# Kernel tuning notes

Measured on AMD Instinct MI355X. Metric: run time of the kernel, lower is better.

The kernel has to match this reference:

```python
import jax, jax.numpy as jnp
import numpy as np


def setup_inputs() -> dict:
    key = jax.random.key(0)
    ks = jax.random.split(key, 11)
    b, c, h, w = 16, 64, 16, 16
    F = 64  # num_filters
    O = 64  # num_outputs
    d_in = 2 * (c + 1)  # 130: concat of two (feature + coord) vectors
    s = 0.05
    return {
        "x_img": jax.random.normal(ks[0], (b, c, h, w), dtype=jnp.float32),
        "Wg0": jax.random.normal(ks[1], (F, d_in), dtype=jnp.float32) * s,
        "bg0": jax.random.normal(ks[2], (F,), dtype=jnp.float32) * s,
        "Wg1": jax.random.normal(ks[3], (F, F), dtype=jnp.float32) * s,
        "bg1": jax.random.normal(ks[4], (F,), dtype=jnp.float32) * s,
        "Wg2": jax.random.normal(ks[5], (F, F), dtype=jnp.float32) * s,
        "bg2": jax.random.normal(ks[6], (F,), dtype=jnp.float32) * s,
        "Wp": jax.random.normal(ks[7], (F, F), dtype=jnp.float32) * s,
        "bp": jax.random.normal(ks[8], (F,), dtype=jnp.float32) * s,
        "Wo": jax.random.normal(ks[9], (O, F), dtype=jnp.float32) * s,
        "bo": jax.random.normal(ks[10], (O,), dtype=jnp.float32) * s,
    }


def reference(x_img, Wg0, bg0, Wg1, bg1, Wg2, bg2, Wp, bp, Wo, bo):
    b, c, h, w = x_img.shape
    L = h * w
    # [b, L, c]: flatten spatial, move channels last
    feats = x_img.reshape(b, c, L).transpose(0, 2, 1)
    # append 1-d coordinate feature -> [b, L, c+1]
    coord = jnp.broadcast_to(
        jnp.arange(L, dtype=feats.dtype).reshape(1, L, 1), (b, L, 1)
    )
    feats = jnp.concatenate([feats, coord], axis=2)
    # pairwise broadcast-concat: pair[b, p, q] = [feats[b, q], feats[b, p]]
    d = feats.shape[-1]
    x_i = jnp.broadcast_to(feats[:, None, :, :], (b, L, L, d))
    x_j = jnp.broadcast_to(feats[:, :, None, :], (b, L, L, d))
    pair = jnp.concatenate([x_i, x_j], axis=3)  # [b, L, L, 2*(c+1)]
    # shared g-MLP (3 layers, ReLU)
    out = jax.nn.relu(jnp.einsum("bpqd,fd->bpqf", pair, Wg0) + bg0)
    out = jax.nn.relu(jnp.einsum("bpqf,gf->bpqg", out, Wg1) + bg1)
    out = jax.nn.relu(jnp.einsum("bpqf,gf->bpqg", out, Wg2) + bg2)
    # sum-reduce over both pair dims -> [b, F]
    out = out.sum(axis=(1, 2))
    # f-network
    out = jax.nn.relu(out @ Wp.T + bp)
    out = out @ Wo.T + bo
    return out
```

## Files before the change

### kernel.cpp

```cpp
#include <hip/hip_runtime.h>


typedef short s8v __attribute__((ext_vector_type(8)));
typedef float f4v __attribute__((ext_vector_type(4)));

#define LDYB 72

__device__ __forceinline__ short bfr(float v) {
  return __builtin_bit_cast(short, (__bf16)v);
}
__device__ __forceinline__ unsigned pkbf(float a, float b) {
  unsigned lo = (unsigned short)__builtin_bit_cast(unsigned short, (__bf16)a);
  unsigned hi = (unsigned short)__builtin_bit_cast(unsigned short, (__bf16)b);
  return lo | (hi << 16);
}
__device__ __forceinline__ f4v relu4(f4v v) {
  f4v z = {0.f, 0.f, 0.f, 0.f};
  return __builtin_elementwise_max(v, z);
}
__device__ __forceinline__ s8v cvt8(f4v a, f4v b) {
  s8v r;
  r[0] = bfr(a[0]); r[1] = bfr(a[1]); r[2] = bfr(a[2]); r[3] = bfr(a[3]);
  r[4] = bfr(b[0]); r[5] = bfr(b[1]); r[6] = bfr(b[2]); r[7] = bfr(b[3]);
  return r;
}
__device__ __forceinline__ f4v ldf4(const float* p) {
  return *(const f4v*)p;
}

__global__ __launch_bounds__(256) void k_pre(
    const float* __restrict__ x, const float* __restrict__ Wg0,
    const float* __restrict__ bg0, float* __restrict__ Ag,
    float* __restrict__ Bg, float* __restrict__ Sg) {
  __shared__ float ws[64 * 131];
  __shared__ float xs[64 * 17];

  const int t = threadIdx.x;
  const int b = blockIdx.x >> 4;
  const int l0 = (blockIdx.x & 15) * 16;

  if (blockIdx.x == 0) {
    for (int i = t; i < 16 * 64; i += 256) Sg[i] = 0.f;
  }
  for (int i = t; i < 64 * 130; i += 256) {
    int f = i / 130, d = i - f * 130;
    ws[f * 131 + d] = Wg0[i];
  }
  for (int i = t; i < 64 * 16; i += 256) {
    int ch = i >> 4, li = i & 15;
    xs[ch * 17 + li] = x[b * 16384 + ch * 256 + l0 + li];
  }
  __syncthreads();

  const int f = t & 63;
  const int w = t >> 6;
  float accA[4] = {0.f, 0.f, 0.f, 0.f};
  float accB[4] = {0.f, 0.f, 0.f, 0.f};
  for (int d = 0; d < 64; ++d) {
    float wa = ws[f * 131 + d];
    float wb = ws[f * 131 + 65 + d];
#pragma unroll
    for (int i = 0; i < 4; ++i) {
      float xv = xs[d * 17 + w + 4 * i];
      accA[i] += xv * wa;
      accB[i] += xv * wb;
    }
  }
  const float wca = ws[f * 131 + 64];
  const float wcb = ws[f * 131 + 129];
  const float bias = bg0[f];
#pragma unroll
  for (int i = 0; i < 4; ++i) {
    int l = l0 + w + 4 * i;
    Ag[(b * 256 + l) * 64 + f] = accA[i] + (float)l * wca;
    Bg[(b * 256 + l) * 64 + f] = accB[i] + (float)l * wcb + bias;
  }
}

__global__ __launch_bounds__(256, 2) void k_main(
    const float* __restrict__ Ag, const float* __restrict__ Bg,
    const float* __restrict__ Wg1, const float* __restrict__ bg1,
    const float* __restrict__ Wg2, const float* __restrict__ bg2,
    float* __restrict__ Sg) {
  __shared__ __align__(16) short Ys[4][16 * LDYB];
  __shared__ float Sblk[64];

  const int t = threadIdx.x;
  const int wid = t >> 6;
  const int lane = t & 63;
  const int mm = lane & 15;
  const int quad = lane >> 4;
  const int b = blockIdx.y;
  const int qg = blockIdx.x & 3;
  const int p0 = (blockIdx.x >> 2) * 32;
  const int q0 = (qg * 4 + wid) * 16;

  if (t < 64) Sblk[t] = 0.f;

  const float* Arow = Ag + (b * 256 + q0 + mm) * 64;
  f4v af0 = ldf4(Arow + quad * 8);
  f4v af1 = ldf4(Arow + quad * 8 + 4);
  f4v af2 = ldf4(Arow + 32 + quad * 8);
  f4v af3 = ldf4(Arow + 36 + quad * 8);

  s8v W1f[4][2], W2f[4][2];
  f4v c1i[4], c2i[4];
#pragma unroll
  for (int gt = 0; gt < 4; ++gt) {
    c1i[gt] = ldf4(bg1 + gt * 16 + quad * 4);
    c2i[gt] = ldf4(bg2 + gt * 16 + quad * 4);
#pragma unroll
    for (int kh = 0; kh < 2; ++kh) {
      const float* r1 = Wg1 + (gt * 16 + mm) * 64 + kh * 32 + quad * 8;
      const float* r2 = Wg2 + (gt * 16 + mm) * 64 + kh * 32 + quad * 8;
      s8v w1, w2;
#pragma unroll
      for (int j = 0; j < 8; ++j) { w1[j] = bfr(r1[j]); w2[j] = bfr(r2[j]); }
      W1f[gt][kh] = w1;
      W2f[gt][kh] = w2;
    }
  }
  __syncthreads();

  short* Yw = Ys[wid];
  const float* Bb = Bg + (b * 256 + p0) * 64;
  f4v cs[4] = {{0.f,0.f,0.f,0.f},{0.f,0.f,0.f,0.f},
               {0.f,0.f,0.f,0.f},{0.f,0.f,0.f,0.f}};

  f4v bq0 = ldf4(Bb + quad * 8);
  f4v bq1 = ldf4(Bb + quad * 8 + 4);
  f4v bq2 = ldf4(Bb + 32 + quad * 8);
  f4v bq3 = ldf4(Bb + 36 + quad * 8);

  for (int ip = 0; ip < 32; ++ip) {
    const float* Bn = Bb + ((ip < 31) ? ip + 1 : 31) * 64;
    f4v bn0 = ldf4(Bn + quad * 8);
    f4v bn1 = ldf4(Bn + quad * 8 + 4);
    f4v bn2 = ldf4(Bn + 32 + quad * 8);
    f4v bn3 = ldf4(Bn + 36 + quad * 8);

    s8v x0 = cvt8(relu4(af0 + bq0), relu4(af1 + bq1));
    s8v x1 = cvt8(relu4(af2 + bq2), relu4(af3 + bq3));

#pragma unroll
    for (int gt = 0; gt < 4; ++gt) {
      f4v a = c1i[gt];
      a = __builtin_amdgcn_mfma_f32_16x16x32_bf16(W1f[gt][0], x0, a, 0, 0, 0);
      a = __builtin_amdgcn_mfma_f32_16x16x32_bf16(W1f[gt][1], x1, a, 0, 0, 0);
      a = relu4(a);
      unsigned d0 = pkbf(a[0], a[1]);
      unsigned d1 = pkbf(a[2], a[3]);
      *(uint2*)&Yw[mm * LDYB + gt * 16 + quad * 4] = make_uint2(d0, d1);
    }

    s8v y0 = *(const s8v*)&Yw[mm * LDYB + quad * 8];
    s8v y1 = *(const s8v*)&Yw[mm * LDYB + 32 + quad * 8];

#pragma unroll
    for (int ot = 0; ot < 4; ++ot) {
      f4v a = c2i[ot];
      a = __builtin_amdgcn_mfma_f32_16x16x32_bf16(W2f[ot][0], y0, a, 0, 0, 0);
      a = __builtin_amdgcn_mfma_f32_16x16x32_bf16(W2f[ot][1], y1, a, 0, 0, 0);
      cs[ot] += relu4(a);
    }

    bq0 = bn0; bq1 = bn1; bq2 = bn2; bq3 = bn3;
  }

#pragma unroll
  for (int ot = 0; ot < 4; ++ot) {
#pragma unroll
    for (int r = 0; r < 4; ++r) {
      float v = cs[ot][r];
      v += __shfl_xor(v, 1);
      v += __shfl_xor(v, 2);
      v += __shfl_xor(v, 4);
      v += __shfl_xor(v, 8);
      if (mm == 0) atomicAdd(&Sblk[ot * 16 + quad * 4 + r], v);
    }
  }
  __syncthreads();
  if (t < 64) atomicAdd(&Sg[b * 64 + t], Sblk[t]);
}

__global__ __launch_bounds__(64) void k_final(
    const float* __restrict__ S, const float* __restrict__ Wp,
    const float* __restrict__ bp, const float* __restrict__ Wo,
    const float* __restrict__ bo, float* __restrict__ out) {
  __shared__ float sv[64], tv[64];
  const int b = blockIdx.x, t = threadIdx.x;
  sv[t] = S[b * 64 + t];
  __syncthreads();
  float acc = bp[t];
  for (int g = 0; g < 64; ++g) acc += sv[g] * Wp[t * 64 + g];
  tv[t] = fmaxf(acc, 0.f);
  __syncthreads();
  float o = bo[t];
  for (int f = 0; f < 64; ++f) o += tv[f] * Wo[t * 64 + f];
  out[b * 64 + t] = o;
}

extern "C" void kernel_launch(void* const* d_in, const int* in_sizes, int n_in,
                              void* d_out, int out_size, void* d_ws, size_t ws_size,
                              hipStream_t stream) {
  const float* x   = (const float*)d_in[0];
  const float* Wg0 = (const float*)d_in[1];
  const float* bg0 = (const float*)d_in[2];
  const float* Wg1 = (const float*)d_in[3];
  const float* bg1 = (const float*)d_in[4];
  const float* Wg2 = (const float*)d_in[5];
  const float* bg2 = (const float*)d_in[6];
  const float* Wp  = (const float*)d_in[7];
  const float* bp  = (const float*)d_in[8];
  const float* Wo  = (const float*)d_in[9];
  const float* bo  = (const float*)d_in[10];
  float* out = (float*)d_out;

  float* Ag = (float*)d_ws;
  float* Bg = Ag + 16 * 256 * 64;
  float* Sg = Bg + 16 * 256 * 64;

  k_pre<<<256, 256, 0, stream>>>(x, Wg0, bg0, Ag, Bg, Sg);
  k_main<<<dim3(32, 16), 256, 0, stream>>>(Ag, Bg, Wg1, bg1, Wg2, bg2, Sg);
  k_final<<<16, 64, 0, stream>>>(Sg, Wp, bp, Wo, bo, out);
}
```

Measured before the change: 119.1 us.

## Halve per-block p range, stage B rows in LDS, raise occupancy

Each k_main block now covers 16 p rows instead of 32, so the grid doubles to 1024 blocks. The block's 16 B rows are loaded once into shared memory and read from LDS inside the loop, replacing the per-iteration global prefetch. Launch bounds rise to 4 blocks per SM to allow more waves in flight, and the weight loads are vectorised. The trade-off is twice the redundant weight/A loading and twice as many global atomics, plus tighter register limits that could cause spills.

```diff
diff --git a/kernel.cpp b/kernel.cpp
--- a/kernel.cpp
+++ b/kernel.cpp
@@ -77,12 +77,13 @@
   }
 }
 
-__global__ __launch_bounds__(256, 2) void k_main(
+__global__ __launch_bounds__(256, 4) void k_main(
     const float* __restrict__ Ag, const float* __restrict__ Bg,
     const float* __restrict__ Wg1, const float* __restrict__ bg1,
     const float* __restrict__ Wg2, const float* __restrict__ bg2,
     float* __restrict__ Sg) {
   __shared__ __align__(16) short Ys[4][16 * LDYB];
+  __shared__ __align__(16) float Bs[16 * 64];
   __shared__ float Sblk[64];
 
   const int t = threadIdx.x;
@@ -91,11 +92,16 @@
   const int mm = lane & 15;
   const int quad = lane >> 4;
   const int b = blockIdx.y;
-  const int qg = blockIdx.x & 3;
-  const int p0 = (blockIdx.x >> 2) * 32;
-  const int q0 = (qg * 4 + wid) * 16;
+  const int qq = blockIdx.x & 3;
+  const int p0 = (blockIdx.x >> 2) * 16;
+  const int q0 = (qq * 4 + wid) * 16;
 
   if (t < 64) Sblk[t] = 0.f;
+
+  {
+    const f4v* Bb4 = (const f4v*)(Bg + (b * 256 + p0) * 64);
+    ((f4v*)Bs)[t] = Bb4[t];
+  }
 
   const float* Arow = Ag + (b * 256 + q0 + mm) * 64;
   f4v af0 = ldf4(Arow + quad * 8);
@@ -113,31 +119,22 @@
     for (int kh = 0; kh < 2; ++kh) {
       const float* r1 = Wg1 + (gt * 16 + mm) * 64 + kh * 32 + quad * 8;
       const float* r2 = Wg2 + (gt * 16 + mm) * 64 + kh * 32 + quad * 8;
-      s8v w1, w2;
-#pragma unroll
-      for (int j = 0; j < 8; ++j) { w1[j] = bfr(r1[j]); w2[j] = bfr(r2[j]); }
-      W1f[gt][kh] = w1;
-      W2f[gt][kh] = w2;
+      W1f[gt][kh] = cvt8(ldf4(r1), ldf4(r1 + 4));
+      W2f[gt][kh] = cvt8(ldf4(r2), ldf4(r2 + 4));
     }
   }
   __syncthreads();
 
   short* Yw = Ys[wid];
-  const float* Bb = Bg + (b * 256 + p0) * 64;
   f4v cs[4] = {{0.f,0.f,0.f,0.f},{0.f,0.f,0.f,0.f},
                {0.f,0.f,0.f,0.f},{0.f,0.f,0.f,0.f}};
 
-  f4v bq0 = ldf4(Bb + quad * 8);
-  f4v bq1 = ldf4(Bb + quad * 8 + 4);
-  f4v bq2 = ldf4(Bb + 32 + quad * 8);
-  f4v bq3 = ldf4(Bb + 36 + quad * 8);
-
-  for (int ip = 0; ip < 32; ++ip) {
-    const float* Bn = Bb + ((ip < 31) ? ip + 1 : 31) * 64;
-    f4v bn0 = ldf4(Bn + quad * 8);
-    f4v bn1 = ldf4(Bn + quad * 8 + 4);
-    f4v bn2 = ldf4(Bn + 32 + quad * 8);
-    f4v bn3 = ldf4(Bn + 36 + quad * 8);
+  for (int ip = 0; ip < 16; ++ip) {
+    const float* brow = &Bs[ip * 64];
+    f4v bq0 = ldf4(brow + quad * 8);
+    f4v bq1 = ldf4(brow + quad * 8 + 4);
+    f4v bq2 = ldf4(brow + 32 + quad * 8);
+    f4v bq3 = ldf4(brow + 36 + quad * 8);
 
     s8v x0 = cvt8(relu4(af0 + bq0), relu4(af1 + bq1));
     s8v x1 = cvt8(relu4(af2 + bq2), relu4(af3 + bq3));
@@ -163,8 +160,6 @@
       a = __builtin_amdgcn_mfma_f32_16x16x32_bf16(W2f[ot][1], y1, a, 0, 0, 0);
       cs[ot] += relu4(a);
     }
-
-    bq0 = bn0; bq1 = bn1; bq2 = bn2; bq3 = bn3;
   }
 
 #pragma unroll
@@ -221,6 +216,6 @@
   float* Sg = Bg + 16 * 256 * 64;
 
   k_pre<<<256, 256, 0, stream>>>(x, Wg0, bg0, Ag, Bg, Sg);
-  k_main<<<dim3(32, 16), 256, 0, stream>>>(Ag, Bg, Wg1, bg1, Wg2, bg2, Sg);
+  k_main<<<dim3(64, 16), 256, 0, stream>>>(Ag, Bg, Wg1, bg1, Wg2, bg2, Sg);
   k_final<<<16, 64, 0, stream>>>(Sg, Wp, bp, Wo, bo, out);
 }
```

Result: slower. 159.4 us (+33.9%).
